# Performance work log

Measured on AMD Instinct MI355X. Metric: run time of the kernel, lower is better.

## Reference

```python
import jax, jax.numpy as jnp
import numpy as np

IN_F = 4096
OUT_F = 4096
GS = 128  # group size for int4 scales


def setup_inputs() -> dict:
    key = jax.random.key(0)
    ks = jax.random.split(key, 5)
    x = jax.random.normal(ks[0], (4, 2048, IN_F), dtype=jnp.float32)
    # each byte packs two unsigned int4 values (low nibble = even col, high nibble = odd col)
    w_packed = jax.random.randint(ks[1], (OUT_F, IN_F // 2), 0, 256, dtype=jnp.int32)
    w_scales = jax.random.uniform(ks[2], (OUT_F, IN_F // GS), dtype=jnp.float32,
                                  minval=0.005, maxval=0.02)
    perm = jax.random.permutation(ks[3], IN_F).astype(jnp.int32)
    bias = jax.random.normal(ks[4], (OUT_F,), dtype=jnp.float32) * 0.01
    return {"x": x, "w_packed": w_packed, "w_scales": w_scales, "perm": perm, "bias": bias}


def _dequantize_groupwise_int4(w_packed, w_scales):
    # unpack two int4 values per byte, zero-point 8 -> symmetric range [-8, 7]
    low = (w_packed & 0xF) - 8
    high = ((w_packed >> 4) & 0xF) - 8
    q = jnp.stack([low, high], axis=-1).reshape(OUT_F, IN_F).astype(jnp.float32)
    # apply one scale per group of GS input features
    w = q.reshape(OUT_F, IN_F // GS, GS) * w_scales[:, :, None]
    return w.reshape(OUT_F, IN_F)  # [out_features, in_features]


def reference(x, w_packed, w_scales, perm, bias):
    shape = x.shape
    xf = x.reshape(-1, IN_F)[:, perm]          # activation permutation (GPTQ act-order)
    w = _dequantize_groupwise_int4(w_packed, w_scales)
    y = xf @ w.T                               # [tokens, out_features]
    return y.reshape(*shape[:-1], OUT_F) + bias
```

## Files before the change

### kernel.cpp

```cpp
#include <hip/hip_runtime.h>

#define IN_F 4096
#define OUT_F 4096
#define GS 128

#define BM 256
#define BN 256
#define BKB 128
#define NT (IN_F / BKB)
#define BUFB (BM * BKB)

typedef int i32x4 __attribute__((ext_vector_type(4)));

typedef __attribute__((address_space(1))) void void_g;
typedef __attribute__((address_space(3))) void void_l;

__device__ __forceinline__ void async_copy16(void* lds, const void* g) {
  __builtin_amdgcn_global_load_lds((const void_g*)g, (void_l*)lds, 16, 0, 0);
}

__device__ __forceinline__ void stage_g(signed char* region, int rowbase,
                                        const signed char* mat, int k0,
                                        int wave, int growl, int gcolb) {
  async_copy16(region + rowbase * BKB + wave * 1024,
               mat + (size_t)(rowbase + growl) * IN_F + k0 + gcolb);
}

__global__ void invperm_kernel(const int* __restrict__ perm, int* __restrict__ inv) {
  int i = blockIdx.x * blockDim.x + threadIdx.x;
  inv[perm[i]] = i;
}

__global__ __launch_bounds__(256) void prep_kernel(
    const float* __restrict__ x,
    unsigned int* __restrict__ xq4,
    float* __restrict__ sx,
    const int* __restrict__ wp,
    const float* __restrict__ wsc,
    const int* __restrict__ inv,
    unsigned int* __restrict__ wq4,
    float* __restrict__ sw,
    int M)
{
  __shared__ unsigned int prow[IN_F / 2];
  __shared__ float srow[IN_F / GS];
  __shared__ float red[256];
  const int tid = threadIdx.x;
  const int b = blockIdx.x;

  if (b < M) {
    const float4* x4 = (const float4*)(x + (size_t)b * IN_F);
    float4 v[4];
    float m = 0.f;
#pragma unroll
    for (int i = 0; i < 4; ++i) {
      v[i] = x4[tid + i * 256];
      m = fmaxf(m, fmaxf(fmaxf(fabsf(v[i].x), fabsf(v[i].y)),
                         fmaxf(fabsf(v[i].z), fabsf(v[i].w))));
    }
    red[tid] = m;
    __syncthreads();
#pragma unroll
    for (int s = 128; s > 0; s >>= 1) {
      if (tid < s) red[tid] = fmaxf(red[tid], red[tid + s]);
      __syncthreads();
    }
    const float mx = red[0];
    const float r = 127.0f / mx;
    if (tid == 0) sx[b] = mx * (1.0f / 127.0f);

    unsigned int* orow = xq4 + (size_t)b * (IN_F / 4);
#pragma unroll
    for (int i = 0; i < 4; ++i) {
      int q0 = (int)rintf(v[i].x * r);
      int q1 = (int)rintf(v[i].y * r);
      int q2 = (int)rintf(v[i].z * r);
      int q3 = (int)rintf(v[i].w * r);
      orow[tid + i * 256] = (unsigned)(q0 & 0xFF) | ((unsigned)(q1 & 0xFF) << 8) |
                            ((unsigned)(q2 & 0xFF) << 16) | ((unsigned)(q3 & 0xFF) << 24);
    }
  } else {
    const int o = b - M;
    const int4* wp4 = (const int4*)(wp + (size_t)o * (IN_F / 2));
    int4* p4 = (int4*)prow;
#pragma unroll
    for (int i = 0; i < 2; ++i)
      p4[tid + i * 256] = wp4[tid + i * 256];
    if (tid < IN_F / GS) srow[tid] = wsc[o * (IN_F / GS) + tid];
    __syncthreads();

    float m = 0.f;
#pragma unroll
    for (int c = 0; c < 8; ++c) {
      const int p = tid + c * 256;
      const unsigned bb = prow[p];
      const float s = srow[p >> 6];
      const float lo = (float)((int)(bb & 0xFu) - 8);
      const float hi = (float)((int)((bb >> 4) & 0xFu) - 8);
      m = fmaxf(m, fmaxf(fabsf(lo), fabsf(hi)) * s);
    }
    red[tid] = m;
    __syncthreads();
#pragma unroll
    for (int s = 128; s > 0; s >>= 1) {
      if (tid < s) red[tid] = fmaxf(red[tid], red[tid + s]);
      __syncthreads();
    }
    const float wmax = red[0];
    const float r = (wmax > 0.f) ? 127.0f / wmax : 0.f;
    if (tid == 0) sw[o] = wmax * (1.0f / 127.0f);

    unsigned int* orow = wq4 + (size_t)o * (IN_F / 4);
    const int4* inv4 = (const int4*)inv;
#pragma unroll
    for (int c = 0; c < 4; ++c) {
      const int p = tid + c * 256;
      const int4 iv = inv4[p];
      unsigned out = 0;
      const int idx[4] = {iv.x, iv.y, iv.z, iv.w};
#pragma unroll
      for (int e = 0; e < 4; ++e) {
        const int ii = idx[e];
        const unsigned wbits = prow[ii >> 1];
        const int n = (int)((wbits >> ((ii & 1) * 4)) & 0xFu) - 8;
        const float v = (float)n * srow[ii >> 7] * r;
        const int q = (int)rintf(v);
        out |= (unsigned)(q & 0xFF) << (e * 8);
      }
      orow[p] = out;
    }
  }
}

template <bool LAST>
__device__ __forceinline__ void gemm_tile(
    const signed char* Ac, const signed char* Bc,
    signed char* An, signed char* Bn,
    const signed char* a_base, const signed char* b_base, int k0n,
    int wave, int wm, int wn, int l16, int quad, int sxz,
    int growl, int gcolb, i32x4 (&acc)[8][4])
{
  i32x4 bq[4][2];
#pragma unroll
  for (int p = 0; p < 4; ++p) {
    if (p == 0) {
#pragma unroll
      for (int j = 0; j < 4; ++j)
#pragma unroll
        for (int ks = 0; ks < 2; ++ks) {
          const int off = (wn + j * 16 + l16) * BKB + ((ks * 64 + quad * 16) ^ sxz);
          bq[j][ks] = *(const i32x4*)(Bc + off);
        }
    }
    i32x4 aq[2][2];
#pragma unroll
    for (int i = 0; i < 2; ++i)
#pragma unroll
      for (int ks = 0; ks < 2; ++ks) {
        const int off = (wm + p * 32 + i * 16 + l16) * BKB + ((ks * 64 + quad * 16) ^ sxz);
        aq[i][ks] = *(const i32x4*)(Ac + off);
      }
    if (!LAST) {
      if (p == 0) {
        stage_g(Bn, 0, b_base, k0n, wave, growl, gcolb);
        stage_g(Bn, 64, b_base, k0n, wave, growl, gcolb);
      } else if (p == 1) {
        stage_g(Bn, 128, b_base, k0n, wave, growl, gcolb);
        stage_g(Bn, 192, b_base, k0n, wave, growl, gcolb);
      } else if (p == 2) {
        stage_g(An, 0, a_base, k0n, wave, growl, gcolb);
        stage_g(An, 128, a_base, k0n, wave, growl, gcolb);
      } else {
        stage_g(An, 64, a_base, k0n, wave, growl, gcolb);
        stage_g(An, 192, a_base, k0n, wave, growl, gcolb);
      }
    }
    __builtin_amdgcn_s_barrier();
    asm volatile("s_waitcnt lgkmcnt(0)" ::: "memory");
    __builtin_amdgcn_sched_barrier(0);
    __builtin_amdgcn_s_setprio(1);
#pragma unroll
    for (int i = 0; i < 2; ++i)
#pragma unroll
      for (int j = 0; j < 4; ++j)
#pragma unroll
        for (int ks = 0; ks < 2; ++ks)
          acc[2 * p + i][j] = __builtin_amdgcn_mfma_i32_16x16x64_i8(
              aq[i][ks], bq[j][ks], acc[2 * p + i][j], 0, 0, 0);
    __builtin_amdgcn_s_setprio(0);
    if (p == 1) {
      if (LAST) { asm volatile("s_waitcnt vmcnt(0)" ::: "memory"); }
      else      { asm volatile("s_waitcnt vmcnt(4)" ::: "memory"); }
      __builtin_amdgcn_sched_barrier(0);
    } else if (p == 3 && !LAST) {
      asm volatile("s_waitcnt vmcnt(2)" ::: "memory");
      __builtin_amdgcn_sched_barrier(0);
    }
    __builtin_amdgcn_s_barrier();
  }
}

__global__ __launch_bounds__(512, 2) void gemm_kernel(
    const signed char* __restrict__ A,
    const signed char* __restrict__ B,
    const float* __restrict__ sx,
    const float* __restrict__ sw,
    const float* __restrict__ bias,
    float* __restrict__ C) {
  __shared__ signed char As[2 * BUFB];
  __shared__ signed char Bs[2 * BUFB];

  const int tid  = threadIdx.x;
  const int wave = tid >> 6;
  const int lane = tid & 63;
  const int quad = lane >> 4;
  const int l16  = lane & 15;

  const int bm = blockIdx.y;
  const int bn = blockIdx.x;
  const signed char* a_base = A + (size_t)bm * BM * IN_F;
  const signed char* b_base = B + (size_t)bn * BN * IN_F;

  const int wm = (wave >> 2) * 128;
  const int wn = (wave & 3) * 64;
  const int sxz = (l16 & 7) << 4;

  const int growl = tid >> 3;
  const int gcolb = ((tid & 7) ^ ((tid >> 3) & 7)) << 4;

  i32x4 acc[8][4] = {};

  stage_g(Bs, 0, b_base, 0, wave, growl, gcolb);
  stage_g(Bs, 64, b_base, 0, wave, growl, gcolb);
  stage_g(Bs, 128, b_base, 0, wave, growl, gcolb);
  stage_g(Bs, 192, b_base, 0, wave, growl, gcolb);
  stage_g(As, 0, a_base, 0, wave, growl, gcolb);
  stage_g(As, 128, a_base, 0, wave, growl, gcolb);
  stage_g(As, 64, a_base, 0, wave, growl, gcolb);
  stage_g(As, 192, a_base, 0, wave, growl, gcolb);
  asm volatile("s_waitcnt vmcnt(2)" ::: "memory");
  __builtin_amdgcn_sched_barrier(0);
  __builtin_amdgcn_s_barrier();

#pragma unroll 1
  for (int t = 0; t < NT - 1; ++t) {
    const int cur = t & 1;
    const int nxt = cur ^ 1;
    gemm_tile<false>(As + cur * BUFB, Bs + cur * BUFB,
                     As + nxt * BUFB, Bs + nxt * BUFB,
                     a_base, b_base, (t + 1) * BKB,
                     wave, wm, wn, l16, quad, sxz, growl, gcolb, acc);
  }
  gemm_tile<true>(As + ((NT - 1) & 1) * BUFB, Bs + ((NT - 1) & 1) * BUFB,
                  nullptr, nullptr, a_base, b_base, 0,
                  wave, wm, wn, l16, quad, sxz, growl, gcolb, acc);

  float* sxs = (float*)As;
  float* sws = sxs + BM;
  float* bsh = sws + BN;
  if (tid < BM) {
    sxs[tid] = sx[bm * BM + tid];
  } else {
    const int c = tid - BM;
    sws[c] = sw[bn * BN + c];
    bsh[c] = bias[bn * BN + c];
  }
  __syncthreads();

  const int wm_g = bm * BM + wm;
  const int wn_g = bn * BN + wn;
#pragma unroll
  for (int j = 0; j < 4; ++j) {
    const int col_l = wn + j * 16 + l16;
    const float swv = sws[col_l];
    const float bv  = bsh[col_l];
    const int col = wn_g + j * 16 + l16;
#pragma unroll
    for (int i = 0; i < 8; ++i) {
      const int row_l0 = wm + i * 16 + quad * 4;
      const int row0 = wm_g + i * 16 + quad * 4;
#pragma unroll
      for (int r = 0; r < 4; ++r)
        C[(size_t)(row0 + r) * OUT_F + col] =
            (float)acc[i][j][r] * (sxs[row_l0 + r] * swv) + bv;
    }
  }
}

extern "C" void kernel_launch(void* const* d_in, const int* in_sizes, int n_in,
                              void* d_out, int out_size, void* d_ws, size_t ws_size,
                              hipStream_t stream) {
  const float* x    = (const float*)d_in[0];
  const int*   wp   = (const int*)d_in[1];
  const float* wsc  = (const float*)d_in[2];
  const int*   perm = (const int*)d_in[3];
  const float* bias = (const float*)d_in[4];
  float* out = (float*)d_out;

  const int M = in_sizes[0] / IN_F;

  signed char* xq = (signed char*)d_ws;
  signed char* wq = xq + (size_t)M * IN_F;
  float* sx = (float*)(wq + (size_t)OUT_F * IN_F);
  float* sw = sx + M;
  int* inv = (int*)(sw + OUT_F);

  invperm_kernel<<<IN_F / 256, 256, 0, stream>>>(perm, inv);

  prep_kernel<<<M + OUT_F, 256, 0, stream>>>(
      x, (unsigned int*)xq, sx, wp, wsc, inv, (unsigned int*)wq, sw, M);

  dim3 grid(OUT_F / BN, M / BM);
  gemm_kernel<<<grid, 512, 0, stream>>>(xq, wq, sx, sw, bias, out);
}
```

Measured before the change: 379.4 us.

## Switch int8 GEMM to 32x32x32 MFMA with register-prefetched LDS fragments

Replaces the 16x16x64 int8 MFMA tiling with 32x32x32 MFMAs, which need fewer LDS fragment loads per unit of math. A operands are now prefetched one phase ahead, including the first fragment of the next tile, so LDS reads overlap the MFMAs. The intra-tile s_barrier before compute is dropped in favour of partial lgkmcnt waits, the global staging order is reshuffled, and output stores become nontemporal. The risks are a correctness hazard from the removed barrier, higher register pressure, and a different epilogue store pattern.

Result: slower. 405.1 us (+6.8%).

```diff
diff --git a/kernel.cpp b/kernel.cpp
--- a/kernel.cpp
+++ b/kernel.cpp
@@ -10,7 +10,8 @@
 #define NT (IN_F / BKB)
 #define BUFB (BM * BKB)
 
-typedef int i32x4 __attribute__((ext_vector_type(4)));
+typedef int i32x4  __attribute__((ext_vector_type(4)));
+typedef int i32x16 __attribute__((ext_vector_type(16)));
 
 typedef __attribute__((address_space(1))) void void_g;
 typedef __attribute__((address_space(3))) void void_l;
@@ -137,62 +138,66 @@
     const signed char* Ac, const signed char* Bc,
     signed char* An, signed char* Bn,
     const signed char* a_base, const signed char* b_base, int k0n,
-    int wave, int wm, int wn, int l16, int quad, int sxz,
-    int growl, int gcolb, i32x4 (&acc)[8][4])
+    int wave, int aoff0, int boff0, const int (&kcs)[4],
+    int growl, int gcolb, i32x4 (&aq)[2][4], i32x4 (&bq)[2][4],
+    i32x16 (&acc)[4][2])
 {
-  i32x4 bq[4][2];
 #pragma unroll
   for (int p = 0; p < 4; ++p) {
     if (p == 0) {
 #pragma unroll
-      for (int j = 0; j < 4; ++j)
-#pragma unroll
-        for (int ks = 0; ks < 2; ++ks) {
-          const int off = (wn + j * 16 + l16) * BKB + ((ks * 64 + quad * 16) ^ sxz);
-          bq[j][ks] = *(const i32x4*)(Bc + off);
-        }
-    }
-    i32x4 aq[2][2];
-#pragma unroll
-    for (int i = 0; i < 2; ++i)
-#pragma unroll
-      for (int ks = 0; ks < 2; ++ks) {
-        const int off = (wm + p * 32 + i * 16 + l16) * BKB + ((ks * 64 + quad * 16) ^ sxz);
-        aq[i][ks] = *(const i32x4*)(Ac + off);
-      }
+      for (int nb = 0; nb < 2; ++nb)
+#pragma unroll
+        for (int ks = 0; ks < 4; ++ks)
+          bq[nb][ks] = *(const i32x4*)(Bc + boff0 + nb * 32 * BKB + kcs[ks]);
+      __builtin_amdgcn_sched_barrier(0);
+#pragma unroll
+      for (int ks = 0; ks < 4; ++ks)
+        aq[0][ks] = *(const i32x4*)(Ac + aoff0 + 1 * 32 * BKB + kcs[ks]);
+    } else if (p == 1) {
+#pragma unroll
+      for (int ks = 0; ks < 4; ++ks)
+        aq[1][ks] = *(const i32x4*)(Ac + aoff0 + 2 * 32 * BKB + kcs[ks]);
+    } else if (p == 2) {
+#pragma unroll
+      for (int ks = 0; ks < 4; ++ks)
+        aq[0][ks] = *(const i32x4*)(Ac + aoff0 + 3 * 32 * BKB + kcs[ks]);
+    } else if (!LAST) {
+#pragma unroll
+      for (int ks = 0; ks < 4; ++ks)
+        aq[1][ks] = *(const i32x4*)(An + aoff0 + 0 * 32 * BKB + kcs[ks]);
+    }
     if (!LAST) {
       if (p == 0) {
         stage_g(Bn, 0, b_base, k0n, wave, growl, gcolb);
         stage_g(Bn, 64, b_base, k0n, wave, growl, gcolb);
       } else if (p == 1) {
+        stage_g(An, 0, a_base, k0n, wave, growl, gcolb);
+        stage_g(An, 128, a_base, k0n, wave, growl, gcolb);
+      } else if (p == 2) {
         stage_g(Bn, 128, b_base, k0n, wave, growl, gcolb);
         stage_g(Bn, 192, b_base, k0n, wave, growl, gcolb);
-      } else if (p == 2) {
-        stage_g(An, 0, a_base, k0n, wave, growl, gcolb);
-        stage_g(An, 128, a_base, k0n, wave, growl, gcolb);
       } else {
         stage_g(An, 64, a_base, k0n, wave, growl, gcolb);
         stage_g(An, 192, a_base, k0n, wave, growl, gcolb);
       }
     }
-    __builtin_amdgcn_s_barrier();
-    asm volatile("s_waitcnt lgkmcnt(0)" ::: "memory");
+    if (p == 3 && LAST) { asm volatile("s_waitcnt lgkmcnt(0)" ::: "memory"); }
+    else                { asm volatile("s_waitcnt lgkmcnt(4)" ::: "memory"); }
     __builtin_amdgcn_sched_barrier(0);
     __builtin_amdgcn_s_setprio(1);
 #pragma unroll
-    for (int i = 0; i < 2; ++i)
-#pragma unroll
-      for (int j = 0; j < 4; ++j)
-#pragma unroll
-        for (int ks = 0; ks < 2; ++ks)
-          acc[2 * p + i][j] = __builtin_amdgcn_mfma_i32_16x16x64_i8(
-              aq[i][ks], bq[j][ks], acc[2 * p + i][j], 0, 0, 0);
+    for (int nb = 0; nb < 2; ++nb)
+#pragma unroll
+      for (int ks = 0; ks < 4; ++ks)
+        acc[p][nb] = __builtin_amdgcn_mfma_i32_32x32x32_i8(
+            aq[(p + 1) & 1][ks], bq[nb][ks], acc[p][nb], 0, 0, 0);
     __builtin_amdgcn_s_setprio(0);
-    if (p == 1) {
+    if (p == 0) {
       if (LAST) { asm volatile("s_waitcnt vmcnt(0)" ::: "memory"); }
-      else      { asm volatile("s_waitcnt vmcnt(4)" ::: "memory"); }
+      else      { asm volatile("s_waitcnt vmcnt(2)" ::: "memory"); }
       __builtin_amdgcn_sched_barrier(0);
-    } else if (p == 3 && !LAST) {
+    } else if ((p == 2 || p == 3) && !LAST) {
       asm volatile("s_waitcnt vmcnt(2)" ::: "memory");
       __builtin_amdgcn_sched_barrier(0);
     }
@@ -207,14 +212,14 @@
     const float* __restrict__ sw,
     const float* __restrict__ bias,
     float* __restrict__ C) {
-  __shared__ signed char As[2 * BUFB];
-  __shared__ signed char Bs[2 * BUFB];
+  __shared__ __align__(16) signed char As[2 * BUFB];
+  __shared__ __align__(16) signed char Bs[2 * BUFB];
 
   const int tid  = threadIdx.x;
   const int wave = tid >> 6;
   const int lane = tid & 63;
-  const int quad = lane >> 4;
-  const int l16  = lane & 15;
+  const int l32  = lane & 31;
+  const int lhi  = lane >> 5;
 
   const int bm = blockIdx.y;
   const int bn = blockIdx.x;
@@ -223,12 +228,20 @@
 
   const int wm = (wave >> 2) * 128;
   const int wn = (wave & 3) * 64;
-  const int sxz = (l16 & 7) << 4;
+
+  const int sxz = (lane & 7) << 4;
+  int kcs[4];
+#pragma unroll
+  for (int ks = 0; ks < 4; ++ks) kcs[ks] = (ks * 32 + lhi * 16) ^ sxz;
+  const int aoff0 = (wm + l32) * BKB;
+  const int boff0 = (wn + l32) * BKB;
 
   const int growl = tid >> 3;
   const int gcolb = ((tid & 7) ^ ((tid >> 3) & 7)) << 4;
 
-  i32x4 acc[8][4] = {};
+  i32x16 acc[4][2] = {};
+  i32x4 aq[2][4];
+  i32x4 bq[2][4];
 
   stage_g(Bs, 0, b_base, 0, wave, growl, gcolb);
   stage_g(Bs, 64, b_base, 0, wave, growl, gcolb);
@@ -242,6 +255,10 @@
   __builtin_amdgcn_sched_barrier(0);
   __builtin_amdgcn_s_barrier();
 
+#pragma unroll
+  for (int ks = 0; ks < 4; ++ks)
+    aq[1][ks] = *(const i32x4*)(As + aoff0 + kcs[ks]);
+
 #pragma unroll 1
   for (int t = 0; t < NT - 1; ++t) {
     const int cur = t & 1;
@@ -249,11 +266,11 @@
     gemm_tile<false>(As + cur * BUFB, Bs + cur * BUFB,
                      As + nxt * BUFB, Bs + nxt * BUFB,
                      a_base, b_base, (t + 1) * BKB,
-                     wave, wm, wn, l16, quad, sxz, growl, gcolb, acc);
+                     wave, aoff0, boff0, kcs, growl, gcolb, aq, bq, acc);
   }
   gemm_tile<true>(As + ((NT - 1) & 1) * BUFB, Bs + ((NT - 1) & 1) * BUFB,
                   nullptr, nullptr, a_base, b_base, 0,
-                  wave, wm, wn, l16, quad, sxz, growl, gcolb, acc);
+                  wave, aoff0, boff0, kcs, growl, gcolb, aq, bq, acc);
 
   float* sxs = (float*)As;
   float* sws = sxs + BM;
@@ -270,19 +287,19 @@
   const int wm_g = bm * BM + wm;
   const int wn_g = bn * BN + wn;
 #pragma unroll
-  for (int j = 0; j < 4; ++j) {
-    const int col_l = wn + j * 16 + l16;
+  for (int nb = 0; nb < 2; ++nb) {
+    const int col_l = wn + nb * 32 + l32;
     const float swv = sws[col_l];
     const float bv  = bsh[col_l];
-    const int col = wn_g + j * 16 + l16;
-#pragma unroll
-    for (int i = 0; i < 8; ++i) {
-      const int row_l0 = wm + i * 16 + quad * 4;
-      const int row0 = wm_g + i * 16 + quad * 4;
-#pragma unroll
-      for (int r = 0; r < 4; ++r)
-        C[(size_t)(row0 + r) * OUT_F + col] =
-            (float)acc[i][j][r] * (sxs[row_l0 + r] * swv) + bv;
+    const int col = wn_g + nb * 32 + l32;
+#pragma unroll
+    for (int mb = 0; mb < 4; ++mb) {
+#pragma unroll
+      for (int r = 0; r < 16; ++r) {
+        const int row_l = wm + mb * 32 + (r & 3) + 8 * (r >> 2) + 4 * lhi;
+        const float val = (float)acc[mb][nb][r] * (sxs[row_l] * swv) + bv;
+        __builtin_nontemporal_store(val, &C[(size_t)(wm_g - wm + row_l) * OUT_F + col]);
+      }
     }
   }
 }
```
